# Optimization experiments

Hardware: AMD Instinct MI355X
Metric: run time of the kernel (lower is better)

The kernel has to match this reference:

```python
import jax, jax.numpy as jnp
import numpy as np
from jax import lax

T, V, E = 8, 10000, 100000
C_IN, H, DS, C_OUT = 128, 256, 16, 64


def setup_inputs() -> dict:
    key = jax.random.key(0)
    ks = jax.random.split(key, 32)
    def nrm(k, shp, s=0.02):
        return jax.random.normal(k, shp, jnp.float32) * s
    inp = {}
    inp['xs'] = jax.random.normal(ks[0], (T, V, C_IN), jnp.float32)
    inp['edge_index'] = jax.random.randint(ks[1], (T, 2, E), 0, V, jnp.int64)
    # pre token mixer: depthwise conv1d over time, kernel 3, pad 1
    inp['w_pre'] = nrm(ks[2], (C_IN, 3), 0.3)
    inp['b_pre'] = jnp.zeros((C_IN,), jnp.float32)
    # per-layer params; layer 0 input C_IN, layer 1 input H
    for i, f in enumerate([C_IN, H]):
        o = 3 + i * 9
        inp[f'w_res{i}'] = nrm(ks[o + 0], (f, H))
        inp[f'b_res{i}'] = jnp.zeros((H,), jnp.float32)
        inp[f'w_self{i}'] = nrm(ks[o + 1], (f, H))
        inp[f'w_neigh{i}'] = nrm(ks[o + 2], (f, H))
        inp[f'b_sage{i}'] = jnp.zeros((H,), jnp.float32)
        inp[f'a_log{i}'] = nrm(ks[o + 3], (H, DS), 0.5)  # Lambda = exp(-exp(a_log)) in (0,1)
        inp[f'B{i}'] = nrm(ks[o + 4], (H, DS), 0.1)
        inp[f'w_mix{i}'] = nrm(ks[o + 5], (H * DS, H))
        inp[f'b_mix{i}'] = jnp.zeros((H,), jnp.float32)
    inp['w_out'] = nrm(ks[25], (H, C_OUT))
    inp['b_out'] = jnp.zeros((C_OUT,), jnp.float32)
    return inp


def _token_mix(xs, w, b):
    # xs: [T, V, C]; depthwise conv over time, kernel 3, zero pad 1
    xp = jnp.pad(xs, ((1, 1), (0, 0), (0, 0)))
    return xp[0:T] * w[:, 0] + xp[1:T + 1] * w[:, 1] + xp[2:T + 2] * w[:, 2] + b


def _sage(x, ei, w_self, w_neigh, b):
    # x: [V, C]; ei: [2, E]; mean aggregation of source features at target nodes
    src, dst = ei[0], ei[1]
    agg = jax.ops.segment_sum(x[src], dst, num_segments=V)          # [V, C]
    deg = jax.ops.segment_sum(jnp.ones((E,), x.dtype), dst, num_segments=V)
    mean = agg / jnp.maximum(deg, 1.0)[:, None]
    return x @ w_self + mean @ w_neigh + b


def _layer(xs, ei, w_res, b_res, w_self, w_neigh, b_sage, a_log, Bp, w_mix, b_mix):
    xsr = xs @ w_res + b_res                                        # [T, V, H]
    h = jax.vmap(_sage, in_axes=(0, 0, None, None, None))(xs, ei, w_self, w_neigh, b_sage)
    lam = jnp.exp(-jnp.exp(a_log))                                  # [H, DS]
    def step(state, x_t):
        state = lam * state + x_t[:, :, None] * Bp                  # [V, H, DS]
        y = jax.nn.relu(state.reshape(V, H * DS)) @ w_mix + b_mix   # [V, H]
        return state, y
    _, ys = lax.scan(step, jnp.zeros((V, H, DS), xs.dtype), h)
    return ys + xsr


def reference(xs, edge_index, w_pre, b_pre,
              w_res0, b_res0, w_self0, w_neigh0, b_sage0, a_log0, B0, w_mix0, b_mix0,
              w_res1, b_res1, w_self1, w_neigh1, b_sage1, a_log1, B1, w_mix1, b_mix1,
              w_out, b_out):
    xs = _token_mix(xs, w_pre, b_pre)
    xs = _layer(xs, edge_index, w_res0, b_res0, w_self0, w_neigh0, b_sage0, a_log0, B0, w_mix0, b_mix0)
    xs = _layer(xs, edge_index, w_res1, b_res1, w_self1, w_neigh1, b_sage1, a_log1, B1, w_mix1, b_mix1)
    return xs[-1] @ w_out + b_out
```

## Files before the change

### kernel.cpp

```cpp
#include <hip/hip_runtime.h>
#include <cstdint>
#include <cstddef>

#define T_DIM 8
#define V_DIM 10000
#define E_DIM 100000
#define M_ALL (T_DIM * V_DIM)

typedef __attribute__((ext_vector_type(8))) short short8;
typedef __attribute__((ext_vector_type(4))) float floatx4;

__device__ __forceinline__ unsigned int f2bf(float f) {
    union { float f; unsigned int u; } v; v.f = f;
    unsigned int u = v.u;
    u = u + 0x7FFFu + ((u >> 16) & 1u);
    return u >> 16;
}
__device__ __forceinline__ float bf2f(unsigned int s) {
    union { unsigned int u; float f; } v; v.u = s << 16;
    return v.f;
}
__device__ __forceinline__ short8 relu8(short8 x) {
    const short8 z = {0,0,0,0,0,0,0,0};
    return __builtin_elementwise_max(x, z);
}
__device__ __forceinline__ unsigned int cvtpk_bf16(float lo, float hi) {
    unsigned int r;
    asm("v_cvt_pk_bf16_f32 %0, %1, %2" : "=v"(r) : "v"(lo), "v"(hi));
    return r;
}
union PK { uint4 u; short8 s; };

__global__ void pack_b_kernel(const float* __restrict__ w, unsigned short* __restrict__ out,
                              int K, int Nw, int NTN_tot, int nt_off, int kt_off) {
    int tid = blockIdx.x * blockDim.x + threadIdx.x;
    int total = (K >> 5) * (Nw >> 4) * 64;
    if (tid >= total) return;
    int lane = tid & 63;
    int f = tid >> 6;
    int ntn_w = Nw >> 4;
    int nt = f % ntn_w;
    int kt = f / ntn_w;
    int kbase = kt * 32 + ((lane >> 4) << 3);
    int n = nt * 16 + (lane & 15);
    unsigned int vals[8];
#pragma unroll
    for (int j = 0; j < 8; ++j)
        vals[j] = f2bf(w[(size_t)(kbase + j) * Nw + n]);
    uint4 pk;
    pk.x = vals[0] | (vals[1] << 16);
    pk.y = vals[2] | (vals[3] << 16);
    pk.z = vals[4] | (vals[5] << 16);
    pk.w = vals[6] | (vals[7] << 16);
    size_t fo = (size_t)(kt + kt_off) * NTN_tot + nt_off + nt;
    *(uint4*)(out + (fo * 64 + lane) * 8) = pk;
}

__global__ void token_mix_kernel(const float* __restrict__ xs, const float* __restrict__ w_pre,
                                 const float* __restrict__ b_pre, unsigned short* __restrict__ ob) {
    const int S = V_DIM * 128;
    int tid = blockIdx.x * blockDim.x + threadIdx.x;
    if (tid >= T_DIM * S / 4) return;
    int e = tid * 4;
    int t = e / S;
    int c = e & 127;
    floatx4 xm = {0.f,0.f,0.f,0.f}, xp = {0.f,0.f,0.f,0.f};
    floatx4 x0 = *(const floatx4*)(xs + e);
    if (t > 0)          xm = *(const floatx4*)(xs + e - S);
    if (t < T_DIM - 1)  xp = *(const floatx4*)(xs + e + S);
    uint2 p; unsigned int b[4];
#pragma unroll
    for (int j = 0; j < 4; ++j) {
        int cc = c + j;
        float r = xm[j]*w_pre[cc*3+0] + x0[j]*w_pre[cc*3+1] + xp[j]*w_pre[cc*3+2] + b_pre[cc];
        b[j] = f2bf(r);
    }
    p.x = b[0] | (b[1] << 16);
    p.y = b[2] | (b[3] << 16);
    *(uint2*)(ob + e) = p;
}

__global__ void lam_kernel(const float* __restrict__ a0, const float* __restrict__ a1,
                           float* __restrict__ lam0, float* __restrict__ lam1) {
    int i = blockIdx.x * blockDim.x + threadIdx.x;
    if (i >= 4096) return;
    lam0[i] = expf(-expf(a0[i]));
    lam1[i] = expf(-expf(a1[i]));
}

__global__ void bias_prep_kernel(const float* __restrict__ bs0, const float* __restrict__ bs1,
                                 const float* __restrict__ bm0, const float* __restrict__ br0,
                                 const float* __restrict__ bm1, const float* __restrict__ br1,
                                 float* __restrict__ bcat0, float* __restrict__ bcat1,
                                 float* __restrict__ bmt0, float* __restrict__ bmt1) {
    int i = blockIdx.x * blockDim.x + threadIdx.x;
    if (i < 512) {
        bcat0[i] = (i < 256) ? bs0[i] : 0.f;
        bcat1[i] = (i < 256) ? bs1[i] : 0.f;
    }
    if (i < 256) {
        bmt0[i] = bm0[i] + br0[i];
        bmt1[i] = bm1[i] + br1[i];
    }
}

__global__ void deg_kernel(const int* __restrict__ ei, int* __restrict__ deg_cnt) {
    int tid = blockIdx.x * blockDim.x + threadIdx.x;
    if (tid >= T_DIM * E_DIM) return;
    int t = tid / E_DIM;
    int e = tid - t * E_DIM;
    int dst = ei[(size_t)t * 2 * E_DIM + E_DIM + e];
    if ((unsigned)dst < V_DIM) atomicAdd(deg_cnt + t * V_DIM + dst, 1);
}

__global__ void invdeg_kernel(const int* __restrict__ deg_cnt, float* __restrict__ inv) {
    int tid = blockIdx.x * blockDim.x + threadIdx.x;
    if (tid >= T_DIM * V_DIM) return;
    inv[tid] = 1.0f / (float)max(deg_cnt[tid], 1);
}

__global__ __launch_bounds__(1024)
void scan_kernel(const int* __restrict__ deg_cnt, int* __restrict__ rowptr) {
    __shared__ int sums[1024];
    int t = blockIdx.x;
    const int* d = deg_cnt + t * V_DIM;
    int* rp = rowptr + t * (V_DIM + 1);
    int tid = threadIdx.x;
    int base = tid * 10;
    int loc[10]; int s = 0;
#pragma unroll
    for (int j = 0; j < 10; ++j) {
        int v = base + j;
        int x = (v < V_DIM) ? d[v] : 0;
        loc[j] = s; s += x;
    }
    sums[tid] = s;
    __syncthreads();
    for (int o = 1; o < 1024; o <<= 1) {
        int v = (tid >= o) ? sums[tid - o] : 0;
        __syncthreads();
        sums[tid] += v;
        __syncthreads();
    }
    int prev = (tid == 0) ? 0 : sums[tid - 1];
#pragma unroll
    for (int j = 0; j < 10; ++j) {
        int v = base + j;
        if (v < V_DIM) rp[v] = prev + loc[j];
    }
    if (tid == 1023) rp[V_DIM] = sums[1023];
}

__global__ void fill_kernel(const int* __restrict__ ei, const int* __restrict__ rowptr,
                            int* __restrict__ fill_cnt, int* __restrict__ srcs) {
    int tid = blockIdx.x * blockDim.x + threadIdx.x;
    if (tid >= T_DIM * E_DIM) return;
    int t = tid / E_DIM;
    int e = tid - t * E_DIM;
    const int* eit = ei + (size_t)t * 2 * E_DIM;
    int src = eit[e];
    int dst = eit[E_DIM + e];
    if ((unsigned)src >= V_DIM || (unsigned)dst >= V_DIM) return;
    int pos = rowptr[t * (V_DIM + 1) + dst] + atomicAdd(fill_cnt + t * V_DIM + dst, 1);
    srcs[(size_t)t * E_DIM + pos] = src;
}

__global__ void gather_pack_kernel(const unsigned short* __restrict__ xn, const int* __restrict__ srcs,
                                   const int* __restrict__ rowptr, const float* __restrict__ invdeg,
                                   const unsigned short* __restrict__ hb,
                                   unsigned short* __restrict__ hpack) {
    int cpx = gridDim.x >> 3;
    int swz = (blockIdx.x & 7) * cpx + (blockIdx.x >> 3);
    int gw = (swz * blockDim.x + threadIdx.x) >> 6;
    int lane = threadIdx.x & 63;
    if (gw >= T_DIM * V_DIM) return;
    int t = gw / V_DIM;
    int v = gw - t * V_DIM;
    const int* rp = rowptr + t * (V_DIM + 1);
    int beg = rp[v], end = rp[v + 1];
    const int* st = srcs + (size_t)t * E_DIM;
    const unsigned short* xnt = xn + (size_t)t * V_DIM * 256;
    float a0 = 0.f, a1 = 0.f, a2 = 0.f, a3 = 0.f;
    for (int i = beg; i < end; ++i) {
        int s = st[i];
        uint2 p = *(const uint2*)(xnt + (size_t)s * 256 + lane * 4);
        a0 += bf2f(p.x & 0xffffu);
        a1 += bf2f(p.x >> 16);
        a2 += bf2f(p.y & 0xffffu);
        a3 += bf2f(p.y >> 16);
    }
    float inv = invdeg[t * V_DIM + v];
    uint2 h = *(const uint2*)(hb + ((size_t)t * V_DIM + v) * 256 + lane * 4);
    a0 = a0 * inv + bf2f(h.x & 0xffffu);
    a1 = a1 * inv + bf2f(h.x >> 16);
    a2 = a2 * inv + bf2f(h.y & 0xffffu);
    a3 = a3 * inv + bf2f(h.y >> 16);
    unsigned short* op = hpack + (size_t)v * 2048 + (size_t)(lane * 4) * 8 + t;
    op[0]  = (unsigned short)f2bf(a0);
    op[8]  = (unsigned short)f2bf(a1);
    op[16] = (unsigned short)f2bf(a2);
    op[24] = (unsigned short)f2bf(a3);
}

template<int KT>
__global__ __launch_bounds__(256, 4)
void gemm_cat2_kernel(const unsigned short* __restrict__ A, const unsigned short* __restrict__ Bp,
                      const float* __restrict__ bias, unsigned short* __restrict__ d_self,
                      unsigned short* __restrict__ d_xn, int M) {
    const int w = threadIdx.x >> 6, lane = threadIdx.x & 63;
    const int quad = lane >> 4, l16 = lane & 15;
    const int region = blockIdx.x;
    const int m0 = blockIdx.y * 64;
    constexpr int K = KT * 32;
    floatx4 acc[4][4];
#pragma unroll
    for (int a = 0; a < 4; ++a)
#pragma unroll
        for (int b = 0; b < 4; ++b) acc[a][b] = (floatx4){0.f,0.f,0.f,0.f};
    const unsigned short* arow[4];
#pragma unroll
    for (int mi = 0; mi < 4; ++mi) {
        int r = m0 + mi * 16 + l16;
        if (r > M - 1) r = M - 1;
        arow[mi] = A + (size_t)r * K + quad * 8;
    }
    const unsigned short* bptr = Bp + ((size_t)(region * 16 + w * 4) * 64 + lane) * 8;
#pragma unroll
    for (int kt = 0; kt < KT; ++kt) {
        short8 bfr[4];
#pragma unroll
        for (int i = 0; i < 4; ++i) bfr[i] = *(const short8*)(bptr + i * 512);
        short8 af[4];
#pragma unroll
        for (int mi = 0; mi < 4; ++mi) af[mi] = *(const short8*)(arow[mi]);
#pragma unroll
        for (int mi = 0; mi < 4; ++mi)
#pragma unroll
            for (int i = 0; i < 4; ++i)
                acc[mi][i] = __builtin_amdgcn_mfma_f32_16x16x32_bf16(af[mi], bfr[i], acc[mi][i], 0, 0, 0);
        bptr += 32 * 512;
#pragma unroll
        for (int mi = 0; mi < 4; ++mi) arow[mi] += 32;
    }
#pragma unroll
    for (int mi = 0; mi < 4; ++mi) {
        int rbase = m0 + mi * 16 + quad * 4;
#pragma unroll
        for (int i = 0; i < 4; ++i) {
            int lcol = w * 64 + i * 16 + l16;
            float b = bias[region * 256 + lcol];
#pragma unroll
            for (int rr = 0; rr < 4; ++rr) {
                int row = rbase + rr;
                if (row < M) {
                    float v = acc[mi][i][rr] + b;
                    size_t off = (size_t)row * 256 + lcol;
                    if (region == 0) d_self[off] = (unsigned short)f2bf(v);
                    else             d_xn[off]  = (unsigned short)f2bf(v);
                }
            }
        }
    }
}

template<int NTC, int KRT>
__global__ __launch_bounds__(256, 4)
void gemm_mix_rec4_kernel(const unsigned short* __restrict__ hp,
                          const unsigned short* __restrict__ Bp,
                          const unsigned short* __restrict__ Ares,
                          const float* __restrict__ lam,
                          const float* __restrict__ Bv,
                          const float* __restrict__ bias,
                          unsigned short* __restrict__ out,
                          int T0base, int OB) {
    constexpr int KR = KRT * 32;
    __shared__ __align__(16) unsigned short Afrag[2][4 * NTC * 64 * 8];
    const int tid = threadIdx.x;
    const int w = tid >> 6, lane = tid & 63;
    const int quad = lane >> 4, l16 = lane & 15;
    const int T0 = T0base + blockIdx.x * NTC;
    const int m0 = blockIdx.y * 16;
    const int prow = tid & 15;
    const int oct  = tid >> 4;
    const int kt_w = oct >> 2, qo = oct & 3;
    const int vr = m0 + prow;

    floatx4 acc[NTC][4];
#pragma unroll
    for (int t = 0; t < NTC; ++t)
#pragma unroll
        for (int i = 0; i < 4; ++i) acc[t][i] = (floatx4){0.f,0.f,0.f,0.f};

    const unsigned short* bptr = Bp + ((size_t)(w * 4) * 64 + lane) * 8;

    auto compute = [&](int ph, int buf) {
        const int kg = ph * 128 + kt_w * 32 + qo * 8;
        const int ch = kg >> 4;
        PK h8; h8.u = *(const uint4*)(hp + (size_t)vr * 2048 + (size_t)ch * 8);
        floatx4 l0 = *(const floatx4*)(lam + kg);
        floatx4 l1 = *(const floatx4*)(lam + kg + 4);
        floatx4 b0 = *(const floatx4*)(Bv + kg);
        floatx4 b1 = *(const floatx4*)(Bv + kg + 4);
        floatx4 sA = {0.f,0.f,0.f,0.f}, sB = {0.f,0.f,0.f,0.f};
        unsigned short* ap = Afrag[buf] + ((size_t)(kt_w * NTC) * 64 + qo * 16 + prow) * 8;
#pragma unroll
        for (int t = 0; t < 8; ++t) {
            float hv = bf2f((unsigned int)(unsigned short)h8.s[t]);
            floatx4 hvv = {hv, hv, hv, hv};
            sA = l0 * sA + hvv * b0;
            sB = l1 * sB + hvv * b1;
            if ((unsigned)(t - T0) < (unsigned)NTC) {
                PK cv;
                cv.u.x = cvtpk_bf16(sA[0], sA[1]);
                cv.u.y = cvtpk_bf16(sA[2], sA[3]);
                cv.u.z = cvtpk_bf16(sB[0], sB[1]);
                cv.u.w = cvtpk_bf16(sB[2], sB[3]);
                PK st; st.s = relu8(cv.s);
                *(uint4*)(ap + (size_t)(t - T0) * 512) = st.u;
            }
        }
    };
    auto consume = [&](int buf) {
#pragma unroll
        for (int kt = 0; kt < 4; ++kt) {
            short8 bfr[4];
#pragma unroll
            for (int i = 0; i < 4; ++i) bfr[i] = *(const short8*)(bptr + i * 512);
            __builtin_amdgcn_s_setprio(1);
#pragma unroll
            for (int ts = 0; ts < NTC; ++ts) {
                short8 af = *(const short8*)(Afrag[buf] + (size_t)((kt * NTC + ts) * 64 + lane) * 8);
#pragma unroll
                for (int i = 0; i < 4; ++i)
                    acc[ts][i] = __builtin_amdgcn_mfma_f32_16x16x32_bf16(af, bfr[i], acc[ts][i], 0, 0, 0);
            }
            __builtin_amdgcn_s_setprio(0);
            bptr += 16 * 512;
        }
    };

    compute(0, 0);
    __syncthreads();
    for (int ph = 0; ph < 32; ++ph) {
        if (ph < 31) compute(ph + 1, (ph + 1) & 1);
        consume(ph & 1);
        __syncthreads();
    }

#pragma unroll
    for (int ktr = 0; ktr < KRT; ++ktr) {
        short8 bfr[4];
#pragma unroll
        for (int i = 0; i < 4; ++i) bfr[i] = *(const short8*)(bptr + i * 512);
#pragma unroll
        for (int ts = 0; ts < NTC; ++ts) {
            const unsigned short* ar = Ares + ((size_t)(T0 + ts) * V_DIM + (size_t)(m0 + l16)) * KR + ktr * 32 + quad * 8;
            short8 af = *(const short8*)ar;
#pragma unroll
            for (int i = 0; i < 4; ++i)
                acc[ts][i] = __builtin_amdgcn_mfma_f32_16x16x32_bf16(af, bfr[i], acc[ts][i], 0, 0, 0);
        }
        bptr += 16 * 512;
    }
#pragma unroll
    for (int ts = 0; ts < NTC; ++ts) {
#pragma unroll
        for (int i = 0; i < 4; ++i) {
            int col = w * 64 + i * 16 + l16;
            float b = bias[col];
#pragma unroll
            for (int rr = 0; rr < 4; ++rr) {
                int row = m0 + quad * 4 + rr;
                out[((size_t)(T0 + ts - OB) * V_DIM + row) * 256 + col] = (unsigned short)f2bf(acc[ts][i][rr] + b);
            }
        }
    }
}

template<int NT, int NTN_TOT, bool RELU>
__global__ __launch_bounds__(512)
void gemm16_kernel(const unsigned short* __restrict__ A, const unsigned short* __restrict__ Bp,
                   const float* __restrict__ bias, float* __restrict__ outF, int M, int K) {
    const int w = threadIdx.x >> 6, lane = threadIdx.x & 63;
    const int quad = lane >> 4, l16 = lane & 15;
    const int rowgrp = w >> 2, nchunk = w & 3;
    const int m0 = blockIdx.x * 32 + rowgrp * 16;
    const int ntb = nchunk * NT;
    constexpr int Ntot = NTN_TOT * 16;
    floatx4 acc[NT];
#pragma unroll
    for (int i = 0; i < NT; ++i) acc[i] = (floatx4){0.f,0.f,0.f,0.f};
    int r = m0 + l16; if (r > M - 1) r = M - 1;
    const unsigned short* arow = A + (size_t)r * K + quad * 8;
    const int ksteps = K >> 5;
    for (int kt = 0; kt < ksteps; ++kt) {
        short8 af = *(const short8*)(arow + kt * 32);
        if (RELU) af = relu8(af);
#pragma unroll
        for (int i = 0; i < NT; ++i) {
            short8 bf = *(const short8*)(Bp + ((size_t)(kt * NTN_TOT + ntb + i) * 64 + lane) * 8);
            acc[i] = __builtin_amdgcn_mfma_f32_16x16x32_bf16(af, bf, acc[i], 0, 0, 0);
        }
    }
    const int rbase = m0 + quad * 4;
#pragma unroll
    for (int i = 0; i < NT; ++i) {
        int col = (ntb + i) * 16 + l16;
        float b = bias[col];
#pragma unroll
        for (int rr = 0; rr < 4; ++rr) {
            int row = rbase + rr;
            if (row < M)
                outF[(size_t)row * Ntot + col] = acc[i][rr] + b;
        }
    }
}

extern "C" void kernel_launch(void* const* d_in, const int* in_sizes, int n_in,
                              void* d_out, int out_size, void* d_ws, size_t ws_size,
                              hipStream_t stream) {
    const float* xs      = (const float*)d_in[0];
    const int*   ei      = (const int*)d_in[1];
    const float* w_pre   = (const float*)d_in[2];
    const float* b_pre   = (const float*)d_in[3];
    const float* w_res0  = (const float*)d_in[4];
    const float* b_res0  = (const float*)d_in[5];
    const float* w_self0 = (const float*)d_in[6];
    const float* w_neigh0= (const float*)d_in[7];
    const float* b_sage0 = (const float*)d_in[8];
    const float* a_log0  = (const float*)d_in[9];
    const float* B0      = (const float*)d_in[10];
    const float* w_mix0  = (const float*)d_in[11];
    const float* b_mix0  = (const float*)d_in[12];
    const float* w_res1  = (const float*)d_in[13];
    const float* b_res1  = (const float*)d_in[14];
    const float* w_self1 = (const float*)d_in[15];
    const float* w_neigh1= (const float*)d_in[16];
    const float* b_sage1 = (const float*)d_in[17];
    const float* a_log1  = (const float*)d_in[18];
    const float* B1      = (const float*)d_in[19];
    const float* w_mix1  = (const float*)d_in[20];
    const float* b_mix1  = (const float*)d_in[21];
    const float* w_out   = (const float*)d_in[22];
    const float* b_out   = (const float*)d_in[23];

    char* wsB = (char*)d_ws;
    size_t off = 0;
    auto alloc = [&](size_t bytes) {
        char* p = wsB + off;
        off += (bytes + 255) & ~(size_t)255;
        return p;
    };
    unsigned short* x0b   = (unsigned short*)alloc((size_t)M_ALL * 128 * 2);
    unsigned short* hA    = (unsigned short*)alloc((size_t)M_ALL * 256 * 2);
    unsigned short* hB    = (unsigned short*)alloc((size_t)M_ALL * 256 * 2);
    unsigned short* hpack = (unsigned short*)alloc((size_t)V_DIM * 2048 * 2);
    unsigned short* x1b   = (unsigned short*)alloc((size_t)M_ALL * 256 * 2);
    unsigned short* out1_b= (unsigned short*)alloc((size_t)V_DIM * 256 * 2);
    int*            deg_cnt = (int*)alloc((size_t)T_DIM * V_DIM * 4);
    float*          invdeg  = (float*)alloc((size_t)T_DIM * V_DIM * 4);
    int*            rowptr  = (int*)alloc((size_t)T_DIM * (V_DIM + 1) * 4);
    int*            fill_cnt= (int*)alloc((size_t)T_DIM * V_DIM * 4);
    int*            srcs    = (int*)alloc((size_t)T_DIM * E_DIM * 4);
    float*          lam0  = (float*)alloc(4096 * 4);
    float*          lam1  = (float*)alloc(4096 * 4);
    float*          bcat0 = (float*)alloc(512 * 4);
    float*          bcat1 = (float*)alloc(512 * 4);
    float*          bmt0  = (float*)alloc(256 * 4);
    float*          bmt1  = (float*)alloc(256 * 4);
    unsigned short* wcat0p= (unsigned short*)alloc((size_t)128 * 512 * 2);
    unsigned short* wcat1p= (unsigned short*)alloc((size_t)256 * 512 * 2);
    unsigned short* wmix0p= (unsigned short*)alloc((size_t)(4096 + 128) * 256 * 2);
    unsigned short* wmix1p= (unsigned short*)alloc((size_t)(4096 + 256) * 256 * 2);
    unsigned short* woutp = (unsigned short*)alloc((size_t)256 * 64 * 2);
    if (off > ws_size) return;

    auto cdiv = [](int a, int b) { return (a + b - 1) / b; };
    const int gMall = cdiv(M_ALL, 64);
    const int gGat  = cdiv(M_ALL * 64, 256);

    lam_kernel<<<16, 256, 0, stream>>>(a_log0, a_log1, lam0, lam1);
    bias_prep_kernel<<<2, 256, 0, stream>>>(b_sage0, b_sage1, b_mix0, b_res0, b_mix1, b_res1,
                                            bcat0, bcat1, bmt0, bmt1);
    pack_b_kernel<<<cdiv(4*16*64, 256), 256, 0, stream>>>(w_self0,  wcat0p, 128, 256, 32, 0, 0);
    pack_b_kernel<<<cdiv(4*16*64, 256), 256, 0, stream>>>(w_neigh0, wcat0p, 128, 256, 32, 16, 0);
    pack_b_kernel<<<cdiv(8*16*64, 256), 256, 0, stream>>>(w_self1,  wcat1p, 256, 256, 32, 0, 0);
    pack_b_kernel<<<cdiv(8*16*64, 256), 256, 0, stream>>>(w_neigh1, wcat1p, 256, 256, 32, 16, 0);
    pack_b_kernel<<<cdiv(128*16*64, 256), 256, 0, stream>>>(w_mix0, wmix0p, 4096, 256, 16, 0, 0);
    pack_b_kernel<<<cdiv(4*16*64, 256),   256, 0, stream>>>(w_res0, wmix0p, 128,  256, 16, 0, 128);
    pack_b_kernel<<<cdiv(128*16*64, 256), 256, 0, stream>>>(w_mix1, wmix1p, 4096, 256, 16, 0, 0);
    pack_b_kernel<<<cdiv(8*16*64, 256),   256, 0, stream>>>(w_res1, wmix1p, 256,  256, 16, 0, 128);
    pack_b_kernel<<<cdiv(8*4*64, 256), 256, 0, stream>>>(w_out, woutp, 256, 64, 4, 0, 0);

    token_mix_kernel<<<cdiv(T_DIM*V_DIM*128/4, 256), 256, 0, stream>>>(xs, w_pre, b_pre, x0b);
    hipMemsetAsync(deg_cnt, 0, (size_t)T_DIM * V_DIM * 4, stream);
    hipMemsetAsync(fill_cnt, 0, (size_t)T_DIM * V_DIM * 4, stream);
    deg_kernel<<<cdiv(T_DIM*E_DIM, 256), 256, 0, stream>>>(ei, deg_cnt);
    scan_kernel<<<T_DIM, 1024, 0, stream>>>(deg_cnt, rowptr);
    invdeg_kernel<<<cdiv(T_DIM*V_DIM, 256), 256, 0, stream>>>(deg_cnt, invdeg);
    fill_kernel<<<cdiv(T_DIM*E_DIM, 256), 256, 0, stream>>>(ei, rowptr, fill_cnt, srcs);

    gemm_cat2_kernel<4><<<dim3(2, gMall), 256, 0, stream>>>(x0b, wcat0p, bcat0, hA, hB, M_ALL);
    gather_pack_kernel<<<gGat, 256, 0, stream>>>(hB, srcs, rowptr, invdeg, hA, hpack);
    gemm_mix_rec4_kernel<4, 4><<<dim3(2, V_DIM / 16), 256, 0, stream>>>(
        hpack, wmix0p, x0b, lam0, B0, bmt0, x1b, 0, 0);

    gemm_cat2_kernel<8><<<dim3(2, gMall), 256, 0, stream>>>(x1b, wcat1p, bcat1, hA, hB, M_ALL);
    gather_pack_kernel<<<gGat, 256, 0, stream>>>(hB, srcs, rowptr, invdeg, hA, hpack);
    gemm_mix_rec4_kernel<1, 8><<<dim3(1, V_DIM / 16), 256, 0, stream>>>(
        hpack, wmix1p, x1b, lam1, B1, bmt1, out1_b, 7, 7);

    gemm16_kernel<1, 4, false><<<cdiv(V_DIM,32), 512, 0, stream>>>(
        out1_b, woutp, b_out, (float*)d_out, V_DIM, 256);
}
```

Baseline: 925.1 us.

## Aggregate neighbor inputs before SAGE GEMM and fuse self/neigh into one K-concat GEMM

Reorders the SAGE computation from mean(x@W_neigh) to mean(x)@W_neigh. The neighbour gather now runs on the narrower input features, and the self and neighbour projections become one GEMM with concatenated K that writes directly into the packed hpack layout. This drops the separate hA/hB intermediates and the bias-concat prep. In exchange the gather output is rounded to bf16 before the GEMM. The epilogue also now uses scattered strided stores with a division per row.

New measurement: 886.1 us. 1.04x faster.

```diff
diff --git a/kernel.cpp b/kernel.cpp
--- a/kernel.cpp
+++ b/kernel.cpp
@@ -88,16 +88,10 @@
     lam1[i] = expf(-expf(a1[i]));
 }
 
-__global__ void bias_prep_kernel(const float* __restrict__ bs0, const float* __restrict__ bs1,
-                                 const float* __restrict__ bm0, const float* __restrict__ br0,
+__global__ void bias_prep_kernel(const float* __restrict__ bm0, const float* __restrict__ br0,
                                  const float* __restrict__ bm1, const float* __restrict__ br1,
-                                 float* __restrict__ bcat0, float* __restrict__ bcat1,
                                  float* __restrict__ bmt0, float* __restrict__ bmt1) {
     int i = blockIdx.x * blockDim.x + threadIdx.x;
-    if (i < 512) {
-        bcat0[i] = (i < 256) ? bs0[i] : 0.f;
-        bcat1[i] = (i < 256) ? bs1[i] : 0.f;
-    }
     if (i < 256) {
         bmt0[i] = bm0[i] + br0[i];
         bmt1[i] = bm1[i] + br1[i];
@@ -165,10 +159,10 @@
     srcs[(size_t)t * E_DIM + pos] = src;
 }
 
-__global__ void gather_pack_kernel(const unsigned short* __restrict__ xn, const int* __restrict__ srcs,
-                                   const int* __restrict__ rowptr, const float* __restrict__ invdeg,
-                                   const unsigned short* __restrict__ hb,
-                                   unsigned short* __restrict__ hpack) {
+template<int CH>
+__global__ void gather_x_kernel(const unsigned short* __restrict__ x, const int* __restrict__ srcs,
+                                const int* __restrict__ rowptr, const float* __restrict__ invdeg,
+                                unsigned short* __restrict__ xm) {
     int cpx = gridDim.x >> 3;
     int swz = (blockIdx.x & 7) * cpx + (blockIdx.x >> 3);
     int gw = (swz * blockDim.x + threadIdx.x) >> 6;
@@ -179,84 +173,89 @@
     const int* rp = rowptr + t * (V_DIM + 1);
     int beg = rp[v], end = rp[v + 1];
     const int* st = srcs + (size_t)t * E_DIM;
-    const unsigned short* xnt = xn + (size_t)t * V_DIM * 256;
-    float a0 = 0.f, a1 = 0.f, a2 = 0.f, a3 = 0.f;
-    for (int i = beg; i < end; ++i) {
-        int s = st[i];
-        uint2 p = *(const uint2*)(xnt + (size_t)s * 256 + lane * 4);
-        a0 += bf2f(p.x & 0xffffu);
-        a1 += bf2f(p.x >> 16);
-        a2 += bf2f(p.y & 0xffffu);
-        a3 += bf2f(p.y >> 16);
-    }
+    const unsigned short* xt = x + (size_t)t * V_DIM * CH;
     float inv = invdeg[t * V_DIM + v];
-    uint2 h = *(const uint2*)(hb + ((size_t)t * V_DIM + v) * 256 + lane * 4);
-    a0 = a0 * inv + bf2f(h.x & 0xffffu);
-    a1 = a1 * inv + bf2f(h.x >> 16);
-    a2 = a2 * inv + bf2f(h.y & 0xffffu);
-    a3 = a3 * inv + bf2f(h.y >> 16);
-    unsigned short* op = hpack + (size_t)v * 2048 + (size_t)(lane * 4) * 8 + t;
-    op[0]  = (unsigned short)f2bf(a0);
-    op[8]  = (unsigned short)f2bf(a1);
-    op[16] = (unsigned short)f2bf(a2);
-    op[24] = (unsigned short)f2bf(a3);
+    if (CH == 128) {
+        float a0 = 0.f, a1 = 0.f;
+        for (int i = beg; i < end; ++i) {
+            int s = st[i];
+            unsigned int p = *(const unsigned int*)(xt + (size_t)s * 128 + lane * 2);
+            a0 += bf2f(p & 0xffffu);
+            a1 += bf2f(p >> 16);
+        }
+        *(unsigned int*)(xm + (size_t)gw * 128 + lane * 2) = cvtpk_bf16(a0 * inv, a1 * inv);
+    } else {
+        float a0 = 0.f, a1 = 0.f, a2 = 0.f, a3 = 0.f;
+        for (int i = beg; i < end; ++i) {
+            int s = st[i];
+            uint2 p = *(const uint2*)(xt + (size_t)s * 256 + lane * 4);
+            a0 += bf2f(p.x & 0xffffu);
+            a1 += bf2f(p.x >> 16);
+            a2 += bf2f(p.y & 0xffffu);
+            a3 += bf2f(p.y >> 16);
+        }
+        uint2 o;
+        o.x = cvtpk_bf16(a0 * inv, a1 * inv);
+        o.y = cvtpk_bf16(a2 * inv, a3 * inv);
+        *(uint2*)(xm + (size_t)gw * 256 + lane * 4) = o;
+    }
 }
 
 template<int KT>
 __global__ __launch_bounds__(256, 4)
-void gemm_cat2_kernel(const unsigned short* __restrict__ A, const unsigned short* __restrict__ Bp,
-                      const float* __restrict__ bias, unsigned short* __restrict__ d_self,
-                      unsigned short* __restrict__ d_xn, int M) {
+void gemm_catf_kernel(const unsigned short* __restrict__ Ax, const unsigned short* __restrict__ Am,
+                      const unsigned short* __restrict__ Bp, const float* __restrict__ bias,
+                      unsigned short* __restrict__ hpack, int M) {
     const int w = threadIdx.x >> 6, lane = threadIdx.x & 63;
     const int quad = lane >> 4, l16 = lane & 15;
-    const int region = blockIdx.x;
-    const int m0 = blockIdx.y * 64;
+    const int m0 = blockIdx.x * 64;
     constexpr int K = KT * 32;
     floatx4 acc[4][4];
 #pragma unroll
     for (int a = 0; a < 4; ++a)
 #pragma unroll
         for (int b = 0; b < 4; ++b) acc[a][b] = (floatx4){0.f,0.f,0.f,0.f};
-    const unsigned short* arow[4];
+    const unsigned short* arowx[4];
+    const unsigned short* arowm[4];
 #pragma unroll
     for (int mi = 0; mi < 4; ++mi) {
         int r = m0 + mi * 16 + l16;
         if (r > M - 1) r = M - 1;
-        arow[mi] = A + (size_t)r * K + quad * 8;
-    }
-    const unsigned short* bptr = Bp + ((size_t)(region * 16 + w * 4) * 64 + lane) * 8;
-#pragma unroll
-    for (int kt = 0; kt < KT; ++kt) {
+        arowx[mi] = Ax + (size_t)r * K + quad * 8;
+        arowm[mi] = Am + (size_t)r * K + quad * 8;
+    }
+    const unsigned short* bptr = Bp + ((size_t)(w * 4) * 64 + lane) * 8;
+#pragma unroll
+    for (int kt = 0; kt < 2 * KT; ++kt) {
         short8 bfr[4];
 #pragma unroll
         for (int i = 0; i < 4; ++i) bfr[i] = *(const short8*)(bptr + i * 512);
         short8 af[4];
 #pragma unroll
-        for (int mi = 0; mi < 4; ++mi) af[mi] = *(const short8*)(arow[mi]);
+        for (int mi = 0; mi < 4; ++mi)
+            af[mi] = (kt < KT) ? *(const short8*)(arowx[mi] + kt * 32)
+                               : *(const short8*)(arowm[mi] + (kt - KT) * 32);
 #pragma unroll
         for (int mi = 0; mi < 4; ++mi)
 #pragma unroll
             for (int i = 0; i < 4; ++i)
                 acc[mi][i] = __builtin_amdgcn_mfma_f32_16x16x32_bf16(af[mi], bfr[i], acc[mi][i], 0, 0, 0);
-        bptr += 32 * 512;
-#pragma unroll
-        for (int mi = 0; mi < 4; ++mi) arow[mi] += 32;
+        bptr += 16 * 512;
     }
 #pragma unroll
     for (int mi = 0; mi < 4; ++mi) {
         int rbase = m0 + mi * 16 + quad * 4;
 #pragma unroll
         for (int i = 0; i < 4; ++i) {
-            int lcol = w * 64 + i * 16 + l16;
-            float b = bias[region * 256 + lcol];
+            int col = w * 64 + i * 16 + l16;
+            float b = bias[col];
 #pragma unroll
             for (int rr = 0; rr < 4; ++rr) {
                 int row = rbase + rr;
                 if (row < M) {
-                    float v = acc[mi][i][rr] + b;
-                    size_t off = (size_t)row * 256 + lcol;
-                    if (region == 0) d_self[off] = (unsigned short)f2bf(v);
-                    else             d_xn[off]  = (unsigned short)f2bf(v);
+                    int t = row / V_DIM;
+                    int v = row - t * V_DIM;
+                    hpack[(size_t)v * 2048 + col * 8 + t] = (unsigned short)f2bf(acc[mi][i][rr] + b);
                 }
             }
         }
@@ -452,8 +451,7 @@
         return p;
     };
     unsigned short* x0b   = (unsigned short*)alloc((size_t)M_ALL * 128 * 2);
-    unsigned short* hA    = (unsigned short*)alloc((size_t)M_ALL * 256 * 2);
-    unsigned short* hB    = (unsigned short*)alloc((size_t)M_ALL * 256 * 2);
+    unsigned short* xm    = (unsigned short*)alloc((size_t)M_ALL * 256 * 2);
     unsigned short* hpack = (unsigned short*)alloc((size_t)V_DIM * 2048 * 2);
     unsigned short* x1b   = (unsigned short*)alloc((size_t)M_ALL * 256 * 2);
     unsigned short* out1_b= (unsigned short*)alloc((size_t)V_DIM * 256 * 2);
@@ -464,28 +462,25 @@
     int*            srcs    = (int*)alloc((size_t)T_DIM * E_DIM * 4);
     float*          lam0  = (float*)alloc(4096 * 4);
     float*          lam1  = (float*)alloc(4096 * 4);
-    float*          bcat0 = (float*)alloc(512 * 4);
-    float*          bcat1 = (float*)alloc(512 * 4);
     float*          bmt0  = (float*)alloc(256 * 4);
     float*          bmt1  = (float*)alloc(256 * 4);
-    unsigned short* wcat0p= (unsigned short*)alloc((size_t)128 * 512 * 2);
-    unsigned short* wcat1p= (unsigned short*)alloc((size_t)256 * 512 * 2);
+    unsigned short* wcat0p= (unsigned short*)alloc((size_t)256 * 256 * 2);
+    unsigned short* wcat1p= (unsigned short*)alloc((size_t)512 * 256 * 2);
     unsigned short* wmix0p= (unsigned short*)alloc((size_t)(4096 + 128) * 256 * 2);
     unsigned short* wmix1p= (unsigned short*)alloc((size_t)(4096 + 256) * 256 * 2);
     unsigned short* woutp = (unsigned short*)alloc((size_t)256 * 64 * 2);
     if (off > ws_size) return;
 
     auto cdiv = [](int a, int b) { return (a + b - 1) / b; };
-    const int gMall = cdiv(M_ALL, 64);
-    const int gGat  = cdiv(M_ALL * 64, 256);
+    const int gMall = M_ALL / 64;
+    const int gGat  = M_ALL / 4;
 
     lam_kernel<<<16, 256, 0, stream>>>(a_log0, a_log1, lam0, lam1);
-    bias_prep_kernel<<<2, 256, 0, stream>>>(b_sage0, b_sage1, b_mix0, b_res0, b_mix1, b_res1,
-                                            bcat0, bcat1, bmt0, bmt1);
-    pack_b_kernel<<<cdiv(4*16*64, 256), 256, 0, stream>>>(w_self0,  wcat0p, 128, 256, 32, 0, 0);
-    pack_b_kernel<<<cdiv(4*16*64, 256), 256, 0, stream>>>(w_neigh0, wcat0p, 128, 256, 32, 16, 0);
-    pack_b_kernel<<<cdiv(8*16*64, 256), 256, 0, stream>>>(w_self1,  wcat1p, 256, 256, 32, 0, 0);
-    pack_b_kernel<<<cdiv(8*16*64, 256), 256, 0, stream>>>(w_neigh1, wcat1p, 256, 256, 32, 16, 0);
+    bias_prep_kernel<<<1, 256, 0, stream>>>(b_mix0, b_res0, b_mix1, b_res1, bmt0, bmt1);
+    pack_b_kernel<<<cdiv(4*16*64, 256), 256, 0, stream>>>(w_self0,  wcat0p, 128, 256, 16, 0, 0);
+    pack_b_kernel<<<cdiv(4*16*64, 256), 256, 0, stream>>>(w_neigh0, wcat0p, 128, 256, 16, 0, 4);
+    pack_b_kernel<<<cdiv(8*16*64, 256), 256, 0, stream>>>(w_self1,  wcat1p, 256, 256, 16, 0, 0);
+    pack_b_kernel<<<cdiv(8*16*64, 256), 256, 0, stream>>>(w_neigh1, wcat1p, 256, 256, 16, 0, 8);
     pack_b_kernel<<<cdiv(128*16*64, 256), 256, 0, stream>>>(w_mix0, wmix0p, 4096, 256, 16, 0, 0);
     pack_b_kernel<<<cdiv(4*16*64, 256),   256, 0, stream>>>(w_res0, wmix0p, 128,  256, 16, 0, 128);
     pack_b_kernel<<<cdiv(128*16*64, 256), 256, 0, stream>>>(w_mix1, wmix1p, 4096, 256, 16, 0, 0);
@@ -500,13 +495,13 @@
     invdeg_kernel<<<cdiv(T_DIM*V_DIM, 256), 256, 0, stream>>>(deg_cnt, invdeg);
     fill_kernel<<<cdiv(T_DIM*E_DIM, 256), 256, 0, stream>>>(ei, rowptr, fill_cnt, srcs);
 
-    gemm_cat2_kernel<4><<<dim3(2, gMall), 256, 0, stream>>>(x0b, wcat0p, bcat0, hA, hB, M_ALL);
-    gather_pack_kernel<<<gGat, 256, 0, stream>>>(hB, srcs, rowptr, invdeg, hA, hpack);
+    gather_x_kernel<128><<<gGat, 256, 0, stream>>>(x0b, srcs, rowptr, invdeg, xm);
+    gemm_catf_kernel<4><<<gMall, 256, 0, stream>>>(x0b, xm, wcat0p, b_sage0, hpack, M_ALL);
     gemm_mix_rec4_kernel<4, 4><<<dim3(2, V_DIM / 16), 256, 0, stream>>>(
         hpack, wmix0p, x0b, lam0, B0, bmt0, x1b, 0, 0);
 
-    gemm_cat2_kernel<8><<<dim3(2, gMall), 256, 0, stream>>>(x1b, wcat1p, bcat1, hA, hB, M_ALL);
-    gather_pack_kernel<<<gGat, 256, 0, stream>>>(hB, srcs, rowptr, invdeg, hA, hpack);
+    gather_x_kernel<256><<<gGat, 256, 0, stream>>>(x1b, srcs, rowptr, invdeg, xm);
+    gemm_catf_kernel<8><<<gMall, 256, 0, stream>>>(x1b, xm, wcat1p, b_sage1, hpack, M_ALL);
     gemm_mix_rec4_kernel<1, 8><<<dim3(1, V_DIM / 16), 256, 0, stream>>>(
         hpack, wmix1p, x1b, lam1, B1, bmt1, out1_b, 7, 7);
 
```
